# Kernel tuning notes

Hardware: AMD Instinct MI355X
Metric: run time of the kernel (lower is better)

Reference implementation:

```python
import jax, jax.numpy as jnp
import numpy as np

B, L, H, V = 256, 2048, 64, 64


def setup_inputs() -> dict:
    key = jax.random.key(0)
    ks = jax.random.split(key, 16)
    s = 0.05
    return {
        "seq": jax.random.randint(ks[0], (B, L), 0, V),
        "embed": jax.random.normal(ks[1], (V, H), jnp.float32) * s,
        "W1": jax.random.normal(ks[2], (2 * H, H), jnp.float32) * s,
        "b1": jnp.zeros((2 * H,), jnp.float32),
        "W2": jax.random.normal(ks[3], (H, 2 * H), jnp.float32) * s,
        "b2": jnp.zeros((H,), jnp.float32),
        "gamma": jnp.ones((H,), jnp.float32),
        "beta": jnp.zeros((H,), jnp.float32),
        "Wk": jax.random.normal(ks[4], (H, H), jnp.float32) * s,
        "Wv": jax.random.normal(ks[5], (H, H), jnp.float32) * s,
        "Wq": jax.random.normal(ks[6], (H, H), jnp.float32) * s,
        "Wrp": jax.random.normal(ks[7], (H, H), jnp.float32) * s,
        "brp": jnp.zeros((H,), jnp.float32),
        "Wout": jax.random.normal(ks[8], (V, H), jnp.float32) * s,
        "bout": jnp.zeros((V,), jnp.float32),
    }


def reference(seq, embed, W1, b1, W2, b2, gamma, beta, Wk, Wv, Wq, Wrp, brp, Wout, bout):
    # encode: LayerNorm(e + FF(e))
    e = embed[seq]                                   # [B, L, H]
    ff = jnp.maximum(e @ W1.T + b1, 0.0) @ W2.T + b2  # [B, L, H]
    h = e + ff
    mu = h.mean(-1, keepdims=True)
    var = ((h - mu) ** 2).mean(-1, keepdims=True)    # torch LN: biased var, eps=1e-5
    hs = (h - mu) / jnp.sqrt(var + 1e-5) * gamma + beta

    # precompute k/v for the first L-1 steps (batched GEMM)
    k_all = hs[:, :-1] @ Wk.T                         # [B, L-1, H]
    v_all = hs[:, :-1] @ Wv.T                         # [B, L-1, H]
    # F.normalize(k, dim=-1): k / max(||k||, 1e-12)
    k_n = k_all / jnp.maximum(jnp.linalg.norm(k_all, axis=-1, keepdims=True), 1e-12)

    def step(M, kv):
        k, v = kv                                      # each [B, H]
        vp = jnp.einsum('bij,bj->bi', M, k)
        M = M + jnp.einsum('bi,bj->bij', v - vp, k)    # rank-1 delta update
        return M, None

    M0 = jnp.zeros((B, H, H), hs.dtype)
    M, _ = jax.lax.scan(step, M0, (jnp.swapaxes(k_n, 0, 1), jnp.swapaxes(v_all, 0, 1)))

    q = hs[:, -1] @ Wq.T                               # [B, H]
    r = jnp.einsum('bij,bj->bi', M, q) @ Wrp.T + brp
    return r @ Wout.T + bout                           # [B, V]
```

## Files before the change

### kernel.cpp

```cpp
#include <hip/hip_runtime.h>


#define DPP_ADD_F32(x, ctrl, rm, bm, bc)                                      \
  (x) = (x) + __int_as_float(__builtin_amdgcn_update_dpp(                     \
            0, __float_as_int(x), (ctrl), (rm), (bm), (bc)))

__device__ __forceinline__ float wave_sum64(float x) {
  DPP_ADD_F32(x, 0x111, 0xf, 0xf, true);
  DPP_ADD_F32(x, 0x112, 0xf, 0xf, true);
  DPP_ADD_F32(x, 0x114, 0xf, 0xf, true);
  DPP_ADD_F32(x, 0x118, 0xf, 0xf, true);
  DPP_ADD_F32(x, 0x142, 0xa, 0xf, false);
  DPP_ADD_F32(x, 0x143, 0xc, 0xf, false);
  return __int_as_float(__builtin_amdgcn_readlane(__float_as_int(x), 63));
}

__device__ __forceinline__ float readlane_f(float x, int lane) {
  return __int_as_float(__builtin_amdgcn_readlane(__float_as_int(x), lane));
}

__global__ __launch_bounds__(64) void build_tables(
    const float* __restrict__ embed, const float* __restrict__ W1,
    const float* __restrict__ b1, const float* __restrict__ W2,
    const float* __restrict__ b2, const float* __restrict__ gamma,
    const float* __restrict__ beta, const float* __restrict__ Wk,
    const float* __restrict__ Wv, const float* __restrict__ Wq,
    float* __restrict__ k_tab, float* __restrict__ v_tab,
    float* __restrict__ q_tab) {
  __shared__ float Wbuf[8448];
  __shared__ float e_s[64];
  __shared__ float f1_s[128];
  __shared__ float hs_s[64];
  const int tok = blockIdx.x;
  const int l = threadIdx.x;

  const float e = embed[tok * 64 + l];
  e_s[l] = e;
#pragma unroll 8
  for (int i = 0; i < 128; ++i) Wbuf[i * 65 + l] = W1[i * 64 + l];
  __syncthreads();

  float a0 = b1[l], a1 = b1[l + 64];
#pragma unroll
  for (int h = 0; h < 64; ++h) {
    a0 = fmaf(e_s[h], Wbuf[l * 65 + h], a0);
    a1 = fmaf(e_s[h], Wbuf[(l + 64) * 65 + h], a1);
  }
  f1_s[l] = fmaxf(a0, 0.f);
  f1_s[l + 64] = fmaxf(a1, 0.f);
  __syncthreads();

#pragma unroll 8
  for (int i = 0; i < 128; ++i)
    Wbuf[(i >> 1) * 131 + (i & 1) * 64 + l] = W2[i * 64 + l];
  __syncthreads();

  float acc = b2[l];
#pragma unroll
  for (int j = 0; j < 128; ++j) acc = fmaf(f1_s[j], Wbuf[l * 131 + j], acc);
  const float hval = e + acc;

  const float mu = wave_sum64(hval) * (1.f / 64.f);
  const float d = hval - mu;
  const float var = wave_sum64(d * d) * (1.f / 64.f);
  const float hs = d * (1.f / sqrtf(var + 1e-5f)) * gamma[l] + beta[l];
  hs_s[l] = hs;
  __syncthreads();

#pragma unroll 8
  for (int i = 0; i < 64; ++i) {
    Wbuf[i * 65 + l] = Wk[i * 64 + l];
    Wbuf[4224 + i * 65 + l] = Wv[i * 64 + l];
  }
  __syncthreads();
  float kk = 0.f, vv = 0.f;
#pragma unroll
  for (int h = 0; h < 64; ++h) {
    kk = fmaf(hs_s[h], Wbuf[l * 65 + h], kk);
    vv = fmaf(hs_s[h], Wbuf[4224 + l * 65 + h], vv);
  }
  __syncthreads();
#pragma unroll 8
  for (int i = 0; i < 64; ++i) Wbuf[i * 65 + l] = Wq[i * 64 + l];
  __syncthreads();
  float qq = 0.f;
#pragma unroll
  for (int h = 0; h < 64; ++h) qq = fmaf(hs_s[h], Wbuf[l * 65 + h], qq);

  float nrm = fmaxf(sqrtf(wave_sum64(kk * kk)), 1e-12f);
  k_tab[tok * 64 + l] = kk / nrm;
  v_tab[tok * 64 + l] = vv;
  q_tab[tok * 64 + l] = qq;
}

__global__ __launch_bounds__(64) void build_gram(
    const float* __restrict__ k_tab, const float* __restrict__ q_tab,
    const float* __restrict__ v_tab, float2* __restrict__ GV,
    float* __restrict__ KQ) {
  __shared__ float k_s[4160];
  __shared__ float q_s[64];
  const int a = blockIdx.x;
  const int l = threadIdx.x;
#pragma unroll 8
  for (int i = 0; i < 64; ++i) k_s[i * 65 + l] = k_tab[i * 64 + l];
  q_s[l] = q_tab[a * 64 + l];
  __syncthreads();
  float g = 0.f, kq = 0.f;
#pragma unroll
  for (int h = 0; h < 64; ++h) {
    g = fmaf(k_s[a * 65 + h], k_s[l * 65 + h], g);
    kq = fmaf(q_s[h], k_s[l * 65 + h], kq);
  }
  GV[a * 64 + l] = make_float2(g, v_tab[a * 64 + l]);
  KQ[a * 64 + l] = kq;
}


#define CHUNK(CONS, PREF, TV, PB)                                             \
  {                                                                           \
    int snxt[16];                                                             \
    _Pragma("unroll") for (int j = 0; j < 16; ++j) snxt[j] =                  \
        __builtin_amdgcn_readlane((TV), (PB) + j);                            \
    _Pragma("unroll") for (int j = 0; j < 16; ++j) PREF[j] =                  \
        GV_s[snxt[j] * 64 + l];                                               \
    _Pragma("unroll") for (int j = 0; j < 16; ++j) {                          \
      const float s = readlane_f(y, ssel[j]);                                 \
      y = fmaf(-s, CONS[j].x, y);                                             \
      r = fmaf(s, CONS[j].y, r);                                              \
    }                                                                         \
    _Pragma("unroll") for (int j = 0; j < 16; ++j) ssel[j] = snxt[j];         \
  }

__global__ __launch_bounds__(64, 1) void scan_head(
    const int* __restrict__ seq, const float2* __restrict__ GVg,
    const float* __restrict__ KQ, const float* __restrict__ Wrp,
    const float* __restrict__ brp, const float* __restrict__ Wout,
    const float* __restrict__ bout, float* __restrict__ out) {
  __shared__ float2 GV_s[4160];
  __shared__ float tmp[64];
  const int b = blockIdx.x;
  const int l = threadIdx.x;

#pragma unroll
  for (int i = 0; i < 32; ++i)
    ((float4*)GV_s)[l + 64 * i] = ((const float4*)GVg)[l + 64 * i];
  GV_s[4096 + l] = make_float2(0.f, 0.f);

  const int* tokp = seq + b * 2048;
  int tok_cur = tokp[2047 - l];
  int tok_nxt = tokp[2047 - 64 - l];
  __syncthreads();

  const int qt = __builtin_amdgcn_readlane(tok_cur, 0);
  float y = KQ[qt * 64 + l];
  float r = 0.f;

  float2 bufA[16], bufB[16];
  int ssel[16];
  {
#pragma unroll
    for (int j = 0; j < 16; ++j)
      ssel[j] = __builtin_amdgcn_readlane(tok_cur, j);
#pragma unroll
    for (int j = 0; j < 16; ++j) bufA[j] = GV_s[ssel[j] * 64 + l];
  }
  bufA[0] = make_float2(0.f, 0.f);

  for (int n = 0; n < 32; ++n) {
    const int tok_fut = (n + 2 <= 31) ? tokp[2047 - 64 * (n + 2) - l] : 0;
    CHUNK(bufA, bufB, tok_cur, 16);
    CHUNK(bufB, bufA, tok_cur, 32);
    CHUNK(bufA, bufB, tok_cur, 48);
    CHUNK(bufB, bufA, tok_nxt, 0);
    tok_cur = tok_nxt;
    tok_nxt = tok_fut;
  }

  float* Wb = (float*)GV_s;
  tmp[l] = r;
#pragma unroll 8
  for (int i = 0; i < 64; ++i) {
    Wb[i * 65 + l] = Wrp[i * 64 + l];
    Wb[4160 + i * 65 + l] = Wout[i * 64 + l];
  }
  __syncthreads();
  float acc = brp[l];
#pragma unroll
  for (int j = 0; j < 64; ++j) acc = fmaf(tmp[j], Wb[l * 65 + j], acc);
  __syncthreads();
  tmp[l] = acc;
  __syncthreads();
  float o = bout[l];
#pragma unroll
  for (int i = 0; i < 64; ++i) o = fmaf(tmp[i], Wb[4160 + l * 65 + i], o);
  out[b * 64 + l] = o;
}

extern "C" void kernel_launch(void* const* d_in, const int* in_sizes, int n_in,
                              void* d_out, int out_size, void* d_ws,
                              size_t ws_size, hipStream_t stream) {
  const int* seq = (const int*)d_in[0];
  const float* embed = (const float*)d_in[1];
  const float* W1 = (const float*)d_in[2];
  const float* b1 = (const float*)d_in[3];
  const float* W2 = (const float*)d_in[4];
  const float* b2 = (const float*)d_in[5];
  const float* gamma = (const float*)d_in[6];
  const float* beta = (const float*)d_in[7];
  const float* Wk = (const float*)d_in[8];
  const float* Wv = (const float*)d_in[9];
  const float* Wq = (const float*)d_in[10];
  const float* Wrp = (const float*)d_in[11];
  const float* brp = (const float*)d_in[12];
  const float* Wout = (const float*)d_in[13];
  const float* bout = (const float*)d_in[14];

  float* wsf = (float*)d_ws;
  float* k_tab = wsf;
  float* v_tab = wsf + 4096;
  float* q_tab = wsf + 8192;
  float2* GV = (float2*)(wsf + 12288);
  float* KQ = wsf + 20480;

  build_tables<<<64, 64, 0, stream>>>(embed, W1, b1, W2, b2, gamma, beta, Wk,
                                      Wv, Wq, k_tab, v_tab, q_tab);
  build_gram<<<64, 64, 0, stream>>>(k_tab, q_tab, v_tab, GV, KQ);
  scan_head<<<256, 64, 0, stream>>>(seq, GV, KQ, Wrp, brp, Wout, bout,
                                    (float*)d_out);
}
```

Baseline: 140.2 us.

## Block the serial readlane scan in groups of four and widen table-build loads

The scan's inner loop previously read y from a lane and updated it one step at a time, so every step waited on the previous readlane. Now steps are processed in groups of four. The Gram cross-terms between the four steps are read up front and the four scalars are solved by a small triangular substitution, which shortens the serial readlane→fma chain. The table and Gram build kernels now use 256 threads so four waves share the cooperative weight loads into shared memory, while wave 0 still does the compute. This adds extra readlanes and FMAs per group in exchange for shorter dependency latency.

```diff
diff --git a/kernel.cpp b/kernel.cpp
--- a/kernel.cpp
+++ b/kernel.cpp
@@ -18,8 +18,9 @@
 __device__ __forceinline__ float readlane_f(float x, int lane) {
   return __int_as_float(__builtin_amdgcn_readlane(__float_as_int(x), lane));
 }
-
-__global__ __launch_bounds__(64) void build_tables(
+#define RLI(v, s) __builtin_amdgcn_readlane((v), (s))
+
+__global__ __launch_bounds__(256) void build_tables(
     const float* __restrict__ embed, const float* __restrict__ W1,
     const float* __restrict__ b1, const float* __restrict__ W2,
     const float* __restrict__ b2, const float* __restrict__ gamma,
@@ -32,103 +33,144 @@
   __shared__ float f1_s[128];
   __shared__ float hs_s[64];
   const int tok = blockIdx.x;
-  const int l = threadIdx.x;
-
-  const float e = embed[tok * 64 + l];
-  e_s[l] = e;
-#pragma unroll 8
-  for (int i = 0; i < 128; ++i) Wbuf[i * 65 + l] = W1[i * 64 + l];
-  __syncthreads();
-
-  float a0 = b1[l], a1 = b1[l + 64];
-#pragma unroll
-  for (int h = 0; h < 64; ++h) {
-    a0 = fmaf(e_s[h], Wbuf[l * 65 + h], a0);
-    a1 = fmaf(e_s[h], Wbuf[(l + 64) * 65 + h], a1);
-  }
-  f1_s[l] = fmaxf(a0, 0.f);
-  f1_s[l + 64] = fmaxf(a1, 0.f);
-  __syncthreads();
-
-#pragma unroll 8
-  for (int i = 0; i < 128; ++i)
-    Wbuf[(i >> 1) * 131 + (i & 1) * 64 + l] = W2[i * 64 + l];
-  __syncthreads();
-
-  float acc = b2[l];
-#pragma unroll
-  for (int j = 0; j < 128; ++j) acc = fmaf(f1_s[j], Wbuf[l * 131 + j], acc);
-  const float hval = e + acc;
-
-  const float mu = wave_sum64(hval) * (1.f / 64.f);
-  const float d = hval - mu;
-  const float var = wave_sum64(d * d) * (1.f / 64.f);
-  const float hs = d * (1.f / sqrtf(var + 1e-5f)) * gamma[l] + beta[l];
-  hs_s[l] = hs;
-  __syncthreads();
-
-#pragma unroll 8
-  for (int i = 0; i < 64; ++i) {
-    Wbuf[i * 65 + l] = Wk[i * 64 + l];
-    Wbuf[4224 + i * 65 + l] = Wv[i * 64 + l];
+  const int tid = threadIdx.x;
+  const int l = tid & 63;
+  const int w = tid >> 6;
+
+  float e = 0.f, hval = 0.f, hs = 0.f;
+#pragma unroll 8
+  for (int i = 0; i < 32; ++i) {
+    const int row = w * 32 + i;
+    Wbuf[row * 65 + l] = W1[row * 64 + l];
+  }
+  if (w == 0) {
+    e = embed[tok * 64 + l];
+    e_s[l] = e;
+  }
+  __syncthreads();
+
+  if (w == 0) {
+    float a0 = b1[l], a1 = b1[l + 64];
+#pragma unroll
+    for (int h = 0; h < 64; ++h) {
+      a0 = fmaf(e_s[h], Wbuf[l * 65 + h], a0);
+      a1 = fmaf(e_s[h], Wbuf[(l + 64) * 65 + h], a1);
+    }
+    f1_s[l] = fmaxf(a0, 0.f);
+    f1_s[l + 64] = fmaxf(a1, 0.f);
+  }
+  __syncthreads();
+
+#pragma unroll 8
+  for (int i = 0; i < 32; ++i) {
+    const int row = w * 32 + i;
+    Wbuf[(row >> 1) * 131 + (row & 1) * 64 + l] = W2[row * 64 + l];
+  }
+  __syncthreads();
+
+  if (w == 0) {
+    float acc = b2[l];
+#pragma unroll
+    for (int j = 0; j < 128; ++j) acc = fmaf(f1_s[j], Wbuf[l * 131 + j], acc);
+    hval = e + acc;
+    const float mu = wave_sum64(hval) * (1.f / 64.f);
+    const float d = hval - mu;
+    const float var = wave_sum64(d * d) * (1.f / 64.f);
+    hs = d * (1.f / sqrtf(var + 1e-5f)) * gamma[l] + beta[l];
+    hs_s[l] = hs;
+  }
+  __syncthreads();
+
+#pragma unroll 8
+  for (int i = 0; i < 16; ++i) {
+    const int row = w * 16 + i;
+    Wbuf[row * 65 + l] = Wk[row * 64 + l];
+    Wbuf[4224 + row * 65 + l] = Wv[row * 64 + l];
   }
   __syncthreads();
   float kk = 0.f, vv = 0.f;
-#pragma unroll
-  for (int h = 0; h < 64; ++h) {
-    kk = fmaf(hs_s[h], Wbuf[l * 65 + h], kk);
-    vv = fmaf(hs_s[h], Wbuf[4224 + l * 65 + h], vv);
-  }
-  __syncthreads();
-#pragma unroll 8
-  for (int i = 0; i < 64; ++i) Wbuf[i * 65 + l] = Wq[i * 64 + l];
-  __syncthreads();
-  float qq = 0.f;
-#pragma unroll
-  for (int h = 0; h < 64; ++h) qq = fmaf(hs_s[h], Wbuf[l * 65 + h], qq);
-
-  float nrm = fmaxf(sqrtf(wave_sum64(kk * kk)), 1e-12f);
-  k_tab[tok * 64 + l] = kk / nrm;
-  v_tab[tok * 64 + l] = vv;
-  q_tab[tok * 64 + l] = qq;
-}
-
-__global__ __launch_bounds__(64) void build_gram(
+  if (w == 0) {
+#pragma unroll
+    for (int h = 0; h < 64; ++h) {
+      kk = fmaf(hs_s[h], Wbuf[l * 65 + h], kk);
+      vv = fmaf(hs_s[h], Wbuf[4224 + l * 65 + h], vv);
+    }
+  }
+  __syncthreads();
+#pragma unroll 8
+  for (int i = 0; i < 16; ++i) {
+    const int row = w * 16 + i;
+    Wbuf[row * 65 + l] = Wq[row * 64 + l];
+  }
+  __syncthreads();
+  if (w == 0) {
+    float qq = 0.f;
+#pragma unroll
+    for (int h = 0; h < 64; ++h) qq = fmaf(hs_s[h], Wbuf[l * 65 + h], qq);
+    float nrm = fmaxf(sqrtf(wave_sum64(kk * kk)), 1e-12f);
+    k_tab[tok * 64 + l] = kk / nrm;
+    v_tab[tok * 64 + l] = vv;
+    q_tab[tok * 64 + l] = qq;
+  }
+}
+
+__global__ __launch_bounds__(256) void build_gram(
     const float* __restrict__ k_tab, const float* __restrict__ q_tab,
     const float* __restrict__ v_tab, float2* __restrict__ GV,
     float* __restrict__ KQ) {
   __shared__ float k_s[4160];
   __shared__ float q_s[64];
   const int a = blockIdx.x;
-  const int l = threadIdx.x;
-#pragma unroll 8
-  for (int i = 0; i < 64; ++i) k_s[i * 65 + l] = k_tab[i * 64 + l];
-  q_s[l] = q_tab[a * 64 + l];
-  __syncthreads();
-  float g = 0.f, kq = 0.f;
-#pragma unroll
-  for (int h = 0; h < 64; ++h) {
-    g = fmaf(k_s[a * 65 + h], k_s[l * 65 + h], g);
-    kq = fmaf(q_s[h], k_s[l * 65 + h], kq);
-  }
-  GV[a * 64 + l] = make_float2(g, v_tab[a * 64 + l]);
-  KQ[a * 64 + l] = kq;
-}
-
-
-#define CHUNK(CONS, PREF, TV, PB)                                             \
-  {                                                                           \
-    int snxt[16];                                                             \
-    _Pragma("unroll") for (int j = 0; j < 16; ++j) snxt[j] =                  \
-        __builtin_amdgcn_readlane((TV), (PB) + j);                            \
-    _Pragma("unroll") for (int j = 0; j < 16; ++j) PREF[j] =                  \
-        GV_s[snxt[j] * 64 + l];                                               \
-    _Pragma("unroll") for (int j = 0; j < 16; ++j) {                          \
-      const float s = readlane_f(y, ssel[j]);                                 \
-      y = fmaf(-s, CONS[j].x, y);                                             \
-      r = fmaf(s, CONS[j].y, r);                                              \
+  const int tid = threadIdx.x;
+  const int l = tid & 63;
+  const int w = tid >> 6;
+#pragma unroll 8
+  for (int i = 0; i < 16; ++i) {
+    const int row = w * 16 + i;
+    k_s[row * 65 + l] = k_tab[row * 64 + l];
+  }
+  if (w == 0) q_s[l] = q_tab[a * 64 + l];
+  __syncthreads();
+  if (w == 0) {
+    float g = 0.f, kq = 0.f;
+#pragma unroll
+    for (int h = 0; h < 64; ++h) {
+      g = fmaf(k_s[a * 65 + h], k_s[l * 65 + h], g);
+      kq = fmaf(q_s[h], k_s[l * 65 + h], kq);
+    }
+    GV[a * 64 + l] = make_float2(g, v_tab[a * 64 + l]);
+    KQ[a * 64 + l] = kq;
+  }
+}
+
+
+#define CHUNK4(CONS, PREF, SC, SP, TV, PB)                                    \
+  _Pragma("unroll") for (int q = 0; q < 4; ++q) {                             \
+    _Pragma("unroll") for (int j = 0; j < 4; ++j) {                           \
+      SP[4 * q + j] = RLI((TV), (PB) + 4 * q + j);                            \
+      PREF[4 * q + j] = GV_s[SP[4 * q + j] * 64 + l];                         \
     }                                                                         \
-    _Pragma("unroll") for (int j = 0; j < 16; ++j) ssel[j] = snxt[j];         \
+    const float T10 = readlane_f(CONS[4 * q + 0].x, SC[4 * q + 1]);           \
+    const float T20 = readlane_f(CONS[4 * q + 0].x, SC[4 * q + 2]);           \
+    const float T30 = readlane_f(CONS[4 * q + 0].x, SC[4 * q + 3]);           \
+    const float T21 = readlane_f(CONS[4 * q + 1].x, SC[4 * q + 2]);           \
+    const float T31 = readlane_f(CONS[4 * q + 1].x, SC[4 * q + 3]);           \
+    const float T32 = readlane_f(CONS[4 * q + 2].x, SC[4 * q + 3]);           \
+    const float s0 = readlane_f(y, SC[4 * q + 0]);                            \
+    const float p1 = readlane_f(y, SC[4 * q + 1]);                            \
+    const float p2 = readlane_f(y, SC[4 * q + 2]);                            \
+    const float p3 = readlane_f(y, SC[4 * q + 3]);                            \
+    const float s1 = fmaf(-s0, T10, p1);                                      \
+    const float s2 = fmaf(-s1, T21, fmaf(-s0, T20, p2));                      \
+    const float s3 = fmaf(-s2, T32, fmaf(-s1, T31, fmaf(-s0, T30, p3)));      \
+    y = fmaf(-s0, CONS[4 * q + 0].x, y);                                      \
+    r = fmaf(s0, CONS[4 * q + 0].y, r);                                       \
+    y = fmaf(-s1, CONS[4 * q + 1].x, y);                                      \
+    r = fmaf(s1, CONS[4 * q + 1].y, r);                                       \
+    y = fmaf(-s2, CONS[4 * q + 2].x, y);                                      \
+    r = fmaf(s2, CONS[4 * q + 2].y, r);                                       \
+    y = fmaf(-s3, CONS[4 * q + 3].x, y);                                      \
+    r = fmaf(s3, CONS[4 * q + 3].y, r);                                       \
   }
 
 __global__ __launch_bounds__(64, 1) void scan_head(
@@ -151,27 +193,25 @@
   int tok_nxt = tokp[2047 - 64 - l];
   __syncthreads();
 
-  const int qt = __builtin_amdgcn_readlane(tok_cur, 0);
+  const int qt = RLI(tok_cur, 0);
   float y = KQ[qt * 64 + l];
   float r = 0.f;
 
   float2 bufA[16], bufB[16];
-  int ssel[16];
-  {
-#pragma unroll
-    for (int j = 0; j < 16; ++j)
-      ssel[j] = __builtin_amdgcn_readlane(tok_cur, j);
-#pragma unroll
-    for (int j = 0; j < 16; ++j) bufA[j] = GV_s[ssel[j] * 64 + l];
+  int sselA[16], sselB[16];
+#pragma unroll
+  for (int j = 0; j < 16; ++j) {
+    sselA[j] = RLI(tok_cur, j);
+    bufA[j] = GV_s[sselA[j] * 64 + l];
   }
   bufA[0] = make_float2(0.f, 0.f);
 
   for (int n = 0; n < 32; ++n) {
     const int tok_fut = (n + 2 <= 31) ? tokp[2047 - 64 * (n + 2) - l] : 0;
-    CHUNK(bufA, bufB, tok_cur, 16);
-    CHUNK(bufB, bufA, tok_cur, 32);
-    CHUNK(bufA, bufB, tok_cur, 48);
-    CHUNK(bufB, bufA, tok_nxt, 0);
+    CHUNK4(bufA, bufB, sselA, sselB, tok_cur, 16);
+    CHUNK4(bufB, bufA, sselB, sselA, tok_cur, 32);
+    CHUNK4(bufA, bufB, sselA, sselB, tok_cur, 48);
+    CHUNK4(bufB, bufA, sselB, sselA, tok_nxt, 0);
     tok_cur = tok_nxt;
     tok_nxt = tok_fut;
   }
@@ -222,9 +262,9 @@
   float2* GV = (float2*)(wsf + 12288);
   float* KQ = wsf + 20480;
 
-  build_tables<<<64, 64, 0, stream>>>(embed, W1, b1, W2, b2, gamma, beta, Wk,
-                                      Wv, Wq, k_tab, v_tab, q_tab);
-  build_gram<<<64, 64, 0, stream>>>(k_tab, q_tab, v_tab, GV, KQ);
+  build_tables<<<64, 256, 0, stream>>>(embed, W1, b1, W2, b2, gamma, beta, Wk,
+                                       Wv, Wq, k_tab, v_tab, q_tab);
+  build_gram<<<64, 256, 0, stream>>>(k_tab, q_tab, v_tab, GV, KQ);
   scan_head<<<256, 64, 0, stream>>>(seq, GV, KQ, Wrp, brp, Wout, bout,
                                     (float*)d_out);
 }
```

Result: slower. 155.3 us (+10.8%).
